# Kernel tuning notes

Measured on AMD Instinct MI355X. Metric: run time of the kernel, lower is better.

The kernel has to match this reference:

```python
import jax, jax.numpy as jnp
import numpy as np

N = 50000          # nodes
E = 400000         # edges
MUL = 32           # multiplicity per irrep
NUM_NEIGHBORS = 8.0
INV_SQRT3 = 1.0 / np.sqrt(3.0)  # w3j(1,1,0) coefficient


def setup_inputs() -> dict:
    key = jax.random.key(0)
    ks = jax.random.split(key, 20)
    inp = {
        # node_input: 32x0e (dim 32) + 32x1o (dim 96) = 128
        "node_input": jax.random.normal(ks[0], (N, 4 * MUL), jnp.float32),
        "node_attr": jnp.ones((N, 1), jnp.float32),           # 1x0e trivial attr
        "edge_src": jax.random.randint(ks[1], (E,), 0, N, jnp.int32),
        "edge_dst": jax.random.randint(ks[2], (E,), 0, N, jnp.int32),
        "edge_attr": jax.random.normal(ks[3], (E, 4), jnp.float32),   # 1x0e + 1x1o
        "edge_scalars": jax.random.normal(ks[4], (E, 16), jnp.float32),
        # FullyConnectedTensorProduct weights (uvw, node_attr has mul 1)
        "w_sc0": jax.random.normal(ks[5], (MUL, MUL), jnp.float32),
        "w_sc1": jax.random.normal(ks[6], (MUL, MUL), jnp.float32),
        "w_lin1_0": jax.random.normal(ks[7], (MUL, MUL), jnp.float32),
        "w_lin1_1": jax.random.normal(ks[8], (MUL, MUL), jnp.float32),
        # radial FC net -> per-edge TP weights (numel = 4*MUL = 128)
        "fc_w1": jax.random.normal(ks[9], (16, 64), jnp.float32),
        "fc_w2": jax.random.normal(ks[10], (64, 4 * MUL), jnp.float32),
        # lin2: irreps_mid (64x0e+64x1o) x attr -> output
        "w_lin2_0": jax.random.normal(ks[11], (2 * MUL, MUL), jnp.float32),
        "w_lin2_1": jax.random.normal(ks[12], (2 * MUL, MUL), jnp.float32),
        # alpha: irreps_mid x attr -> 0e (zero-init in original; small randn for a nontrivial test)
        "w_alpha": 0.1 * jax.random.normal(ks[13], (2 * MUL, 1), jnp.float32),
        # sc_edges: irreps_mid x edge_attr -> edge_attr
        "w_se0a": jax.random.normal(ks[14], (2 * MUL,), jnp.float32),  # mid0e x ea0e -> 0e
        "w_se0b": jax.random.normal(ks[15], (2 * MUL,), jnp.float32),  # mid1o x ea1o -> 0e
        "w_se1a": jax.random.normal(ks[16], (2 * MUL,), jnp.float32),  # mid0e x ea1o -> 1o
        "w_se1b": jax.random.normal(ks[17], (2 * MUL,), jnp.float32),  # mid1o x ea0e -> 1o
    }
    return inp


def reference(node_input, node_attr, edge_src, edge_dst, edge_attr, edge_scalars,
              w_sc0, w_sc1, w_lin1_0, w_lin1_1, fc_w1, fc_w2,
              w_lin2_0, w_lin2_1, w_alpha, w_se0a, w_se0b, w_se1a, w_se1b):
    inv_nn = 1.0 / jnp.sqrt(jnp.asarray(NUM_NEIGHBORS, node_input.dtype))
    n = node_input.shape[0]
    x0 = node_input[:, :MUL]                       # (N, 32)   32x0e
    x1 = node_input[:, MUL:].reshape(n, MUL, 3)    # (N, 32, 3) 32x1o
    a = node_attr                                  # (N, 1)
    s_in = 1.0 / np.sqrt(MUL)                      # FCTP fan-in normalization

    # self-connection: FCTP(input, attr) -> output
    sc0 = (x0 @ w_sc0) * a * s_in
    sc1 = jnp.einsum('num,uw->nwm', x1, w_sc1) * a[:, :, None] * s_in
    node_self = jnp.concatenate([sc0, sc1.reshape(n, 3 * MUL)], axis=1)  # (N, 128)

    # lin1: FCTP(input, attr) -> input irreps
    f0 = (x0 @ w_lin1_0) * a * s_in
    f1 = jnp.einsum('num,uw->nwm', x1, w_lin1_1) * a[:, :, None] * s_in

    # gather source node features per edge
    g0 = f0[edge_src]                              # (E, 32)
    g1 = f1[edge_src]                              # (E, 32, 3)
    ea0 = edge_attr[:, :1]                         # (E, 1)   1x0e
    ea1 = edge_attr[:, 1:]                         # (E, 3)   1x1o

    # radial net -> per-edge TP weights (FullyConnectedNet with sin activation)
    h = jnp.sin(edge_scalars @ fc_w1 * (1.0 / np.sqrt(16.0)))
    w = h @ fc_w2 * (1.0 / np.sqrt(64.0))          # (E, 128)
    wA, wB, wC, wD = jnp.split(w, 4, axis=1)       # each (E, 32)

    # uvu tensor product, 4 instructions
    mA = wA * g0 * ea0                                           # 0e x 0e -> 0e
    mD = wD * jnp.einsum('eum,em->eu', g1, ea1) * INV_SQRT3      # 1o x 1o -> 0e
    mB = (wB * g0)[:, :, None] * ea1[:, None, :]                 # 0e x 1o -> 1o
    mC = (wC[:, :, None] * g1) * ea0[:, :, None]                 # 1o x 0e -> 1o
    mid0 = jnp.concatenate([mA, mD], axis=1)       # (E, 64)  64x0e
    mid1 = jnp.concatenate([mB, mC], axis=1)       # (E, 64, 3) 64x1o

    # scatter-add to destination nodes
    n0 = jax.ops.segment_sum(mid0, edge_dst, num_segments=n) * inv_nn
    n1 = jax.ops.segment_sum(mid1, edge_dst, num_segments=n) * inv_nn

    s_mid = 1.0 / np.sqrt(2 * MUL)
    out0 = (n0 @ w_lin2_0) * a * s_mid
    out1 = jnp.einsum('num,uw->nwm', n1, w_lin2_1) * a[:, :, None] * s_mid
    node_conv = jnp.concatenate([out0, out1.reshape(n, 3 * MUL)], axis=1)

    # alpha gate (sc.output_mask is all ones here, so alpha = 1 - 1 + alpha*1)
    alpha = (n0 @ w_alpha) * a * s_mid             # (N, 1)
    node_conv_out = node_self + alpha * node_conv  # (N, 128)

    # sc_edges: FCTP(mid, edge_attr) -> edge_attr irreps; fan-in = 128 per output
    s_se = 1.0 / np.sqrt(4 * MUL)
    se0 = ((mid0 @ w_se0a) * ea0[:, 0]
           + jnp.einsum('eum,em,u->e', mid1, ea1, w_se0b) * INV_SQRT3) * s_se
    se1 = ((mid0 @ w_se1a)[:, None] * ea1
           + jnp.einsum('eum,u->em', mid1, w_se1b) * ea0) * s_se
    edge_conv_out = edge_attr + jnp.concatenate([se0[:, None], se1], axis=1) * inv_nn

    return node_conv_out, edge_conv_out
```

## Files before the change

kernel.cpp:

```cpp
#include <hip/hip_runtime.h>
#include <math.h>

#define N_NODES 50000
#define E_EDGES 400000
#define NPRE_BLOCKS 6250
#define NHIST_BLOCKS 1563
#define NEDGE_BLOCKS 6250

typedef _Float16 f16x2 __attribute__((ext_vector_type(2)));
typedef _Float16 f16x4 __attribute__((ext_vector_type(4)));
typedef _Float16 f16x8 __attribute__((ext_vector_type(8)));
typedef float    f32x4 __attribute__((ext_vector_type(4)));

static constexpr float S_IN      = 0.17677669529663687f;
static constexpr float S_MID     = 0.125f;
static constexpr float S_SE      = 0.08838834764831843f;
static constexpr float INV_NN    = 0.35355339059327373f;
static constexpr float INV_SQRT3 = 0.5773502691896258f;
static constexpr float FC1_S     = 0.25f;
static constexpr float FC2_S     = 0.125f;

#define WAVE_LDS_FENCE() asm volatile("s_waitcnt lgkmcnt(0)" ::: "memory")

__device__ inline float wave_reduce_dpp(float v) {
    int x;
    x = __builtin_amdgcn_update_dpp(0, __float_as_int(v), 0x111, 0xf, 0xf, true); v += __int_as_float(x);
    x = __builtin_amdgcn_update_dpp(0, __float_as_int(v), 0x112, 0xf, 0xf, true); v += __int_as_float(x);
    x = __builtin_amdgcn_update_dpp(0, __float_as_int(v), 0x114, 0xf, 0xf, true); v += __int_as_float(x);
    x = __builtin_amdgcn_update_dpp(0, __float_as_int(v), 0x118, 0xf, 0xf, true); v += __int_as_float(x);
    x = __builtin_amdgcn_update_dpp(0, __float_as_int(v), 0x142, 0xa, 0xf, true); v += __int_as_float(x);
    x = __builtin_amdgcn_update_dpp(0, __float_as_int(v), 0x143, 0xc, 0xf, true); v += __int_as_float(x);
    return __int_as_float(__builtin_amdgcn_readlane(__float_as_int(v), 63));
}

__global__ __launch_bounds__(256) void pre_hist_kernel(
    const float* __restrict__ node_input, const float* __restrict__ node_attr,
    const float* __restrict__ w_sc0, const float* __restrict__ w_sc1,
    const float* __restrict__ w_lin1_0, const float* __restrict__ w_lin1_1,
    float* __restrict__ out_self, _Float16* __restrict__ ws_h,
    const int* __restrict__ edge_dst, int* __restrict__ counts,
    const float* __restrict__ edge_scalars, _Float16* __restrict__ ES_h,
    float* __restrict__ nacc)
{
    const int t = threadIdx.x;
    if (blockIdx.x >= NPRE_BLOCKS) {
        const int e = (blockIdx.x - NPRE_BLOCKS) * 256 + t;
        if (e < E_EDGES) {
            atomicAdd(&counts[edge_dst[e]], 1);
            const float4* s4 = (const float4*)edge_scalars + (size_t)e * 4;
            _Float16* dp = ES_h + (size_t)e * 16;
            #pragma unroll
            for (int i = 0; i < 4; ++i) {
                const float4 v = s4[i];
                f16x4 p = {(_Float16)v.x, (_Float16)v.y, (_Float16)v.z, (_Float16)v.w};
                *(f16x4*)&dp[i * 4] = p;
            }
        }
        return;
    }
    const int n0 = blockIdx.x * 8;
    __shared__ __align__(16) float sx[8 * 128];
    __shared__ float sa[8];
    {
        const int k = t >> 5, q = t & 31;
        const float4 v = ((const float4*)(node_input + (size_t)n0 * 128))[t];
        if (q < 8) {
            *(float4*)&sx[k * 128 + q * 4] = v;
        } else {
            const int base = q * 4 - 32;
            const float vv[4] = {v.x, v.y, v.z, v.w};
            #pragma unroll
            for (int j = 0; j < 4; ++j) {
                const int uj = (base + j) / 3, mj = (base + j) % 3;
                sx[k * 128 + 32 + mj * 32 + uj] = vv[j];
            }
        }
    }
    {
        float4* nz = (float4*)(nacc + (size_t)n0 * 256);
        const float4 z4 = {0.f, 0.f, 0.f, 0.f};
        nz[t] = z4; nz[t + 256] = z4;
    }
    if (t < 8) sa[t] = node_attr[n0 + t];
    __syncthreads();

    const int half = t >> 7;
    const int idx  = t & 127;
    float wcol[32];
    int xoff = 0;
    if (idx < 32) {
        const float* __restrict__ W = half ? w_lin1_0 : w_sc0;
        #pragma unroll
        for (int u = 0; u < 32; ++u) wcol[u] = W[u * 32 + idx];
    } else {
        const float* __restrict__ W = half ? w_lin1_1 : w_sc1;
        const int j = idx - 32;
        const int w = j / 3; const int m = j % 3;
        xoff = 32 + m * 32;
        #pragma unroll
        for (int u = 0; u < 32; ++u) wcol[u] = W[u * 32 + w];
    }
    #pragma unroll
    for (int k = 0; k < 8; ++k) {
        const float* xb = sx + k * 128 + xoff;
        float acc = 0.f;
        #pragma unroll
        for (int u4 = 0; u4 < 8; ++u4) {
            const f32x4 xv = *(const f32x4*)&xb[u4 * 4];
            acc += xv[0] * wcol[u4 * 4 + 0];
            acc += xv[1] * wcol[u4 * 4 + 1];
            acc += xv[2] * wcol[u4 * 4 + 2];
            acc += xv[3] * wcol[u4 * 4 + 3];
        }
        const float v = acc * sa[k] * S_IN;
        if (half) ws_h[(size_t)(n0 + k) * 128 + idx] = (_Float16)v;
        else      out_self[(size_t)(n0 + k) * 128 + idx] = v;
    }
}

__global__ __launch_bounds__(1024) void scan_block_kernel(
    const int* __restrict__ counts, int* __restrict__ cursor, int* __restrict__ bsum,
    const float* __restrict__ fc_w1, const float* __restrict__ fc_w2,
    const float* __restrict__ w_se0a, const float* __restrict__ w_se0b,
    const float* __restrict__ w_se1a, const float* __restrict__ w_se1b,
    _Float16* __restrict__ W2T_g, _Float16* __restrict__ W1T_g,
    _Float16* __restrict__ BT_g)
{
    const int t = threadIdx.x;
    if (blockIdx.x == 49) {
        for (int u = t; u < 8192; u += 1024) {
            const int k = u >> 7, c = u & 127;
            W2T_g[c * 72 + k] = (_Float16)fc_w2[u];
        }
        {
            W2T_g[(t >> 3) * 72 + 64 + (t & 7)] = (_Float16)0.f;
        }
        {
            const int j = t >> 4, k = t & 15;
            W1T_g[t] = (_Float16)fc_w1[k * 64 + j];
        }
        for (int u = t; u < 2112; u += 1024) BT_g[u] = (_Float16)0.f;
        __syncthreads();
        if (t < 256) {
            const int uu = t & 63, p = t >> 6;
            const float ev = (p == 0) ? w_se0a[uu] : w_se1b[uu];
            const float ov = (p == 0) ? w_se1a[uu] : w_se0b[uu];
            BT_g[(2 * p) * 264 + 4 * uu + p]     = (_Float16)ev;
            BT_g[(2 * p + 1) * 264 + 4 * uu + p] = (_Float16)ov;
        }
        return;
    }
    const int idx = blockIdx.x * 1024 + t;
    const int c   = (idx < N_NODES) ? counts[idx] : 0;
    int v = c, x;
    x = __builtin_amdgcn_update_dpp(0, v, 0x111, 0xf, 0xf, true); v += x;
    x = __builtin_amdgcn_update_dpp(0, v, 0x112, 0xf, 0xf, true); v += x;
    x = __builtin_amdgcn_update_dpp(0, v, 0x114, 0xf, 0xf, true); v += x;
    x = __builtin_amdgcn_update_dpp(0, v, 0x118, 0xf, 0xf, true); v += x;
    x = __builtin_amdgcn_update_dpp(0, v, 0x142, 0xa, 0xf, true); v += x;
    x = __builtin_amdgcn_update_dpp(0, v, 0x143, 0xc, 0xf, true); v += x;
    __shared__ int swv[16], sex[16];
    const int wid = t >> 6;
    if ((t & 63) == 63) swv[wid] = v;
    __syncthreads();
    if (t < 16) {
        int a = 0;
        for (int j = 0; j < t; ++j) a += swv[j];
        sex[t] = a;
        if (t == 15) bsum[blockIdx.x] = a + swv[15];
    }
    __syncthreads();
    if (idx < N_NODES) cursor[idx] = v - c + sex[wid];
}

__global__ __launch_bounds__(1024) void scan_fixup_kernel(
    int* __restrict__ cursor, const int* __restrict__ bsum)
{
    __shared__ int boff_s;
    const int t = threadIdx.x;
    if (t < 64) {
        int v = (t < (int)blockIdx.x) ? bsum[t] : 0;
        #pragma unroll
        for (int off = 32; off >= 1; off >>= 1) v += __shfl_down(v, off, 64);
        if (t == 0) boff_s = v;
    }
    __syncthreads();
    const int idx = blockIdx.x * 1024 + t;
    if (idx < N_NODES) cursor[idx] += boff_s;
}

__global__ __launch_bounds__(256) void scatter_kernel(
    const int* __restrict__ edge_dst, int* __restrict__ cursor,
    int* __restrict__ sorted_eid)
{
    const int e = blockIdx.x * 256 + threadIdx.x;
    if (e < E_EDGES) {
        const int p = atomicAdd(&cursor[edge_dst[e]], 1);
        sorted_eid[p] = e;
    }
}

__global__ __launch_bounds__(256, 5) void edge_kernel(
    const _Float16* __restrict__ ws_h,
    const int* __restrict__ edge_src, const int* __restrict__ edge_dst,
    const float* __restrict__ edge_attr, const _Float16* __restrict__ ES_h,
    const _Float16* __restrict__ W2T_g, const _Float16* __restrict__ W1T_g,
    const _Float16* __restrict__ BT_g,
    const int* __restrict__ sorted_eid,
    float* __restrict__ nacc, float* __restrict__ edge_out)
{
    __shared__ __align__(16) _Float16 sArena[13056];
    __shared__ __align__(16) float sDep[4][36];

    _Float16* __restrict__ sHT = sArena;
    _Float16* __restrict__ sWt = sArena + 4608;

    const int t    = threadIdx.x;
    const int lane = t & 63;
    const int wv   = t >> 6;
    const int quad = lane >> 4;
    const int mm   = lane & 15;

    const int orig = blockIdx.x;
    const int xcd  = orig & 7;
    constexpr int q = NEDGE_BLOCKS >> 3, r = NEDGE_BLOCKS & 7;
    const int bid = (xcd < r ? xcd * (q + 1) : r * (q + 1) + (xcd - r) * q) + (orig >> 3);
    const int e0 = bid * 64;
    const int eb = wv * 16;

    int eidreg = 0, srcreg = 0, dstreg = 0;
    float4 ear = {0.f, 0.f, 0.f, 0.f};
    if (lane < 16) {
        eidreg = sorted_eid[e0 + eb + lane];
        srcreg = edge_src[eidreg];
        dstreg = edge_dst[eidreg];
        ear    = ((const float4*)edge_attr)[eidreg];
    }

    f16x8 a_w1[4];
    f16x8 b_es = {};
    if (quad < 2) {
        const int myeid = __shfl(eidreg, mm);
        b_es = *(const f16x8*)&ES_h[(size_t)myeid * 16 + quad * 8];
        #pragma unroll
        for (int jt = 0; jt < 4; ++jt)
            a_w1[jt] = *(const f16x8*)&W1T_g[(jt * 16 + mm) * 16 + quad * 8];
    } else {
        #pragma unroll
        for (int jt = 0; jt < 4; ++jt) a_w1[jt] = (f16x8){};
    }

    const bool hi = lane >= 32;
    const int  u  = lane - 32;
    const int idxA = hi ? (32 + 3 * u) : lane;
    const int idxB = hi ? (33 + 3 * u) : lane;
    const int idxC = hi ? (34 + 3 * u) : lane;
    const int col1 = hi ? (96 + u) : lane;
    const int col2 = hi ? (64 + u) : (32 + lane);

    float ga[2][4], gb[2][4], gc[2][4];
    #pragma unroll
    for (int b = 0; b < 2; ++b)
        #pragma unroll
        for (int i = 0; i < 4; ++i) {
            const int s = __shfl(srcreg, b * 4 + i);
            const _Float16* fr = ws_h + (size_t)s * 128;
            ga[b][i] = (float)fr[idxA];
            gb[b][i] = (float)fr[idxB];
            gc[b][i] = (float)fr[idxC];
        }
    asm volatile("" ::: "memory");

    #pragma unroll
    for (int jt = 0; jt < 4; ++jt) {
        f32x4 d = {0.f, 0.f, 0.f, 0.f};
        d = __builtin_amdgcn_mfma_f32_16x16x32_f16(a_w1[jt], b_es, d, 0, 0, 0);
        f16x4 hv;
        hv[0] = (_Float16)__sinf(d[0] * FC1_S);
        hv[1] = (_Float16)__sinf(d[1] * FC1_S);
        hv[2] = (_Float16)__sinf(d[2] * FC1_S);
        hv[3] = (_Float16)__sinf(d[3] * FC1_S);
        *(f16x4*)&sHT[(eb + mm) * 72 + jt * 16 + quad * 4] = hv;
    }
    WAVE_LDS_FENCE();

    f32x4 dacc[8];
    {
        const f16x8 b_lo = *(const f16x8*)&sHT[(eb + mm) * 72 + quad * 8];
        const f16x8 b_hi = *(const f16x8*)&sHT[(eb + mm) * 72 + 32 + quad * 8];
        #pragma unroll
        for (int ct = 0; ct < 8; ++ct) {
            const f16x8 a_lo = *(const f16x8*)&W2T_g[(ct * 16 + mm) * 72 + quad * 8];
            const f16x8 a_hi = *(const f16x8*)&W2T_g[(ct * 16 + mm) * 72 + 32 + quad * 8];
            f32x4 d = {0.f, 0.f, 0.f, 0.f};
            d = __builtin_amdgcn_mfma_f32_16x16x32_f16(a_lo, b_lo, d, 0, 0, 0);
            d = __builtin_amdgcn_mfma_f32_16x16x32_f16(a_hi, b_hi, d, 0, 0, 0);
            dacc[ct] = d;
        }
    }

    #pragma unroll
    for (int ct = 0; ct < 8; ++ct) {
        f16x4 v;
        v[0] = (_Float16)(dacc[ct][0] * FC2_S);
        v[1] = (_Float16)(dacc[ct][1] * FC2_S);
        v[2] = (_Float16)(dacc[ct][2] * FC2_S);
        v[3] = (_Float16)(dacc[ct][3] * FC2_S);
        *(f16x4*)&sWt[(eb + mm) * 132 + ct * 16 + quad * 4] = v;
    }
    WAVE_LDS_FENCE();

    int   cur = -1;
    float am0 = 0.f, axx = 0.f, ayy = 0.f, azz = 0.f;
    _Float16* __restrict__ myA = sArena + wv * 1152;
    const _Float16* __restrict__ arow = myA + (mm & 3) * 264;
    const _Float16* __restrict__ btrow = BT_g + (mm & 7) * 264;

    #pragma unroll
    for (int b = 0; b < 4; ++b) {
        const int sl = b & 1;
        float w1b[4], w2b[4];
        #pragma unroll
        for (int i = 0; i < 4; ++i) {
            w1b[i] = (float)sWt[(eb + b * 4 + i) * 132 + col1];
            w2b[i] = (float)sWt[(eb + b * 4 + i) * 132 + col2];
        }
        #pragma unroll
        for (int i = 0; i < 4; ++i) {
            const int el = b * 4 + i;
            const int dst = __shfl(dstreg, el);
            const float ea0 = __shfl(ear.x, el);
            const float e1x = __shfl(ear.y, el);
            const float e1y = __shfl(ear.z, el);
            const float e1z = __shfl(ear.w, el);
            const float w1v = w1b[i];
            const float w2v = w2b[i];

            float mid0, m1x, m1y, m1z;
            if (!hi) {
                mid0 = w1v * ga[sl][i] * ea0;
                const float wbg = w2v * ga[sl][i];
                m1x = wbg * e1x; m1y = wbg * e1y; m1z = wbg * e1z;
            } else {
                const float dot = ga[sl][i] * e1x + gb[sl][i] * e1y + gc[sl][i] * e1z;
                mid0 = w1v * dot * INV_SQRT3;
                const float wce = w2v * ea0;
                m1x = wce * ga[sl][i]; m1y = wce * gb[sl][i]; m1z = wce * gc[sl][i];
            }

            if (dst != cur) {
                if (cur >= 0) {
                    float* np_ = nacc + (size_t)cur * 256;
                    atomicAdd(np_ + lane, am0);
                    atomicAdd(np_ + 64 + lane, axx);
                    atomicAdd(np_ + 128 + lane, ayy);
                    atomicAdd(np_ + 192 + lane, azz);
                }
                cur = dst; am0 = axx = ayy = azz = 0.f;
            }
            am0 += mid0; axx += m1x; ayy += m1y; azz += m1z;

            f16x4 mv;
            mv[0] = (_Float16)mid0; mv[1] = (_Float16)m1x;
            mv[2] = (_Float16)m1y;  mv[3] = (_Float16)m1z;
            *(f16x4*)&myA[i * 264 + 4 * lane] = mv;
        }

        if (b < 2) {
            #pragma unroll
            for (int i = 0; i < 4; ++i) {
                const int s = __shfl(srcreg, (b + 2) * 4 + i);
                const _Float16* fr = ws_h + (size_t)s * 128;
                ga[sl][i] = (float)fr[idxA];
                gb[sl][i] = (float)fr[idxB];
                gc[sl][i] = (float)fr[idxC];
            }
            asm volatile("" ::: "memory");
        }

        f32x4 d = {0.f, 0.f, 0.f, 0.f};
        #pragma unroll
        for (int ks = 0; ks < 8; ++ks) {
            const f16x8 a  = *(const f16x8*)&arow[ks * 32 + quad * 8];
            const f16x8 bb = *(const f16x8*)&btrow[ks * 32 + quad * 8];
            d = __builtin_amdgcn_mfma_f32_16x16x32_f16(a, bb, d, 0, 0, 0);
        }
        if (lane < 8) {
            float4 f4; f4.x = d[0]; f4.y = d[1]; f4.z = d[2]; f4.w = d[3];
            *(float4*)&sDep[wv][lane * 4] = f4;
        }
        const int oeid = __shfl(eidreg, b * 4 + (lane & 3));
        const float oea0 = __shfl(ear.x, b * 4 + (lane & 3));
        const float oe1x = __shfl(ear.y, b * 4 + (lane & 3));
        const float oe1y = __shfl(ear.z, b * 4 + (lane & 3));
        const float oe1z = __shfl(ear.w, b * 4 + (lane & 3));
        if (lane < 4) {
            const float c0 = sDep[wv][ 0 + lane], c1 = sDep[wv][ 4 + lane];
            const float c2 = sDep[wv][ 8 + lane], c3 = sDep[wv][12 + lane];
            const float c4 = sDep[wv][16 + lane], c5 = sDep[wv][20 + lane];
            const float c6 = sDep[wv][24 + lane], c7 = sDep[wv][28 + lane];
            const float s0 = c0 * oea0 + (c3 * oe1x + c5 * oe1y + c7 * oe1z) * INV_SQRT3;
            float4 o;
            o.x = oea0 + s0 * S_SE * INV_NN;
            o.y = oe1x + (c1 * oe1x + c2 * oea0) * S_SE * INV_NN;
            o.z = oe1y + (c1 * oe1y + c4 * oea0) * S_SE * INV_NN;
            o.w = oe1z + (c1 * oe1z + c6 * oea0) * S_SE * INV_NN;
            *(float4*)&edge_out[(size_t)oeid * 4] = o;
        }
    }
    if (cur >= 0) {
        float* np_ = nacc + (size_t)cur * 256;
        atomicAdd(np_ + lane, am0);
        atomicAdd(np_ + 64 + lane, axx);
        atomicAdd(np_ + 128 + lane, ayy);
        atomicAdd(np_ + 192 + lane, azz);
    }
}

__global__ __launch_bounds__(128) void node_post_kernel(
    const float* __restrict__ nacc, const float* __restrict__ node_attr,
    const float* __restrict__ w_lin2_0, const float* __restrict__ w_lin2_1,
    const float* __restrict__ w_alpha, float* __restrict__ out)
{
    const int n0 = blockIdx.x * 8, t = threadIdx.x;
    __shared__ __align__(16) float sn[8 * 256];
    __shared__ float salpha[8];
    const float4* src = (const float4*)(nacc + (size_t)n0 * 256);
    #pragma unroll
    for (int i = 0; i < 4; ++i) ((float4*)sn)[t + i * 128] = src[t + i * 128];
    __syncthreads();

    if (t < 64) {
        const float wa = w_alpha[t];
        #pragma unroll
        for (int k = 0; k < 8; ++k) {
            const float r = wave_reduce_dpp(sn[k * 256 + t] * wa);
            if (t == 0) salpha[k] = r;
        }
    }
    __syncthreads();

    float wcol[64];
    int xoff = 0;
    if (t < 32) {
        #pragma unroll
        for (int u = 0; u < 64; ++u) wcol[u] = w_lin2_0[u * 32 + t];
    } else {
        const int j = t - 32; const int w = j / 3; const int m = j % 3;
        xoff = 64 + m * 64;
        #pragma unroll
        for (int u = 0; u < 64; ++u) wcol[u] = w_lin2_1[u * 32 + w];
    }
    #pragma unroll
    for (int k = 0; k < 8; ++k) {
        const float* xb = sn + k * 256 + xoff;
        float acc = 0.f;
        #pragma unroll
        for (int u4 = 0; u4 < 16; ++u4) {
            const f32x4 xv = *(const f32x4*)&xb[u4 * 4];
            acc += xv[0] * wcol[u4 * 4 + 0];
            acc += xv[1] * wcol[u4 * 4 + 1];
            acc += xv[2] * wcol[u4 * 4 + 2];
            acc += xv[3] * wcol[u4 * 4 + 3];
        }
        const float a  = node_attr[n0 + k];
        const float sc = a * S_MID * INV_NN;
        const size_t o = (size_t)(n0 + k) * 128 + t;
        out[o] = out[o] + (salpha[k] * sc) * (acc * sc);
    }
}

extern "C" void kernel_launch(void* const* d_in, const int* in_sizes, int n_in,
                              void* d_out, int out_size, void* d_ws, size_t ws_size,
                              hipStream_t stream)
{
    const float* node_input   = (const float*)d_in[0];
    const float* node_attr    = (const float*)d_in[1];
    const int*   edge_src     = (const int*)d_in[2];
    const int*   edge_dst     = (const int*)d_in[3];
    const float* edge_attr    = (const float*)d_in[4];
    const float* edge_scalars = (const float*)d_in[5];
    const float* w_sc0        = (const float*)d_in[6];
    const float* w_sc1        = (const float*)d_in[7];
    const float* w_lin1_0     = (const float*)d_in[8];
    const float* w_lin1_1     = (const float*)d_in[9];
    const float* fc_w1        = (const float*)d_in[10];
    const float* fc_w2        = (const float*)d_in[11];
    const float* w_lin2_0     = (const float*)d_in[12];
    const float* w_lin2_1     = (const float*)d_in[13];
    const float* w_alpha      = (const float*)d_in[14];
    const float* w_se0a       = (const float*)d_in[15];
    const float* w_se0b       = (const float*)d_in[16];
    const float* w_se1a       = (const float*)d_in[17];
    const float* w_se1b       = (const float*)d_in[18];

    float* out      = (float*)d_out;
    float* edge_out = out + (size_t)N_NODES * 128;

    _Float16* ws_h = (_Float16*)d_ws;
    _Float16* ES_h = ws_h + (size_t)N_NODES * 128;
    float* nacc   = (float*)((char*)d_ws + (size_t)N_NODES * 128 * 4);
    int*   counts = (int*)(nacc + (size_t)N_NODES * 256);
    int*   cursor = counts + N_NODES;
    int*   sid    = cursor + N_NODES;
    int*   bsum   = sid + E_EDGES;
    _Float16* W2T_g = (_Float16*)(bsum + 64);
    _Float16* W1T_g = W2T_g + 9216;
    _Float16* BT_g  = W1T_g + 1024;

    hipMemsetAsync(counts, 0, N_NODES * sizeof(int), stream);

    pre_hist_kernel<<<NPRE_BLOCKS + NHIST_BLOCKS, 256, 0, stream>>>(
        node_input, node_attr, w_sc0, w_sc1, w_lin1_0, w_lin1_1, out, ws_h,
        edge_dst, counts, edge_scalars, ES_h, nacc);

    scan_block_kernel<<<50, 1024, 0, stream>>>(counts, cursor, bsum,
        fc_w1, fc_w2, w_se0a, w_se0b, w_se1a, w_se1b, W2T_g, W1T_g, BT_g);
    scan_fixup_kernel<<<49, 1024, 0, stream>>>(cursor, bsum);
    scatter_kernel<<<(E_EDGES + 255) / 256, 256, 0, stream>>>(edge_dst, cursor, sid);

    edge_kernel<<<NEDGE_BLOCKS, 256, 0, stream>>>(
        ws_h, edge_src, edge_dst, edge_attr, ES_h, W2T_g, W1T_g, BT_g,
        sid, nacc, edge_out);

    node_post_kernel<<<N_NODES / 8, 128, 0, stream>>>(
        nacc, node_attr, w_lin2_0, w_lin2_1, w_alpha, out);
}
```

Measured before the change: 373.2 us.

## Fuse scan, fixup and scatter into one kernel with grid-wide barriers

Replaces the three counting-sort kernels (block scan, scan fixup, scatter) with one persistent kernel of 128 blocks that uses atomic-counter grid barriers between phases. The aim is to remove two kernel launches and their inter-kernel gaps. The scatter phase becomes a grid-stride loop over 128×1024 threads. This relies on all 128 blocks being co-resident, otherwise the barrier deadlocks. It also raises the edge_kernel occupancy hint from 5 to 6 waves per SIMD, which may increase register pressure or spilling.

```diff
diff --git a/kernel.cpp b/kernel.cpp
--- a/kernel.cpp
+++ b/kernel.cpp
@@ -6,6 +6,7 @@
 #define NPRE_BLOCKS 6250
 #define NHIST_BLOCKS 1563
 #define NEDGE_BLOCKS 6250
+#define NFUSE_BLOCKS 128
 
 typedef _Float16 f16x2 __attribute__((ext_vector_type(2)));
 typedef _Float16 f16x4 __attribute__((ext_vector_type(4)));
@@ -33,6 +34,17 @@
     return __int_as_float(__builtin_amdgcn_readlane(__float_as_int(v), 63));
 }
 
+__device__ inline void gsync(int* cnt, int target) {
+    __syncthreads();
+    if (threadIdx.x == 0) {
+        __hip_atomic_fetch_add(cnt, 1, __ATOMIC_ACQ_REL, __HIP_MEMORY_SCOPE_AGENT);
+        while (__hip_atomic_load(cnt, __ATOMIC_ACQUIRE, __HIP_MEMORY_SCOPE_AGENT) < target)
+            __builtin_amdgcn_s_sleep(8);
+    }
+    __syncthreads();
+    __threadfence();
+}
+
 __global__ __launch_bounds__(256) void pre_hist_kernel(
     const float* __restrict__ node_input, const float* __restrict__ node_attr,
     const float* __restrict__ w_sc0, const float* __restrict__ w_sc1,
@@ -40,9 +52,10 @@
     float* __restrict__ out_self, _Float16* __restrict__ ws_h,
     const int* __restrict__ edge_dst, int* __restrict__ counts,
     const float* __restrict__ edge_scalars, _Float16* __restrict__ ES_h,
-    float* __restrict__ nacc)
+    float* __restrict__ nacc, int* __restrict__ sync_cnt)
 {
     const int t = threadIdx.x;
+    if (blockIdx.x == 0 && t == 0) *sync_cnt = 0;
     if (blockIdx.x >= NPRE_BLOCKS) {
         const int e = (blockIdx.x - NPRE_BLOCKS) * 256 + t;
         if (e < E_EDGES) {
@@ -118,16 +131,43 @@
     }
 }
 
-__global__ __launch_bounds__(1024) void scan_block_kernel(
-    const int* __restrict__ counts, int* __restrict__ cursor, int* __restrict__ bsum,
+__global__ __launch_bounds__(1024) void sort_fused_kernel(
+    const int* __restrict__ edge_dst, const int* __restrict__ counts,
+    int* __restrict__ cursor, int* __restrict__ bsum,
+    int* __restrict__ sorted_eid, int* __restrict__ sync_cnt,
     const float* __restrict__ fc_w1, const float* __restrict__ fc_w2,
     const float* __restrict__ w_se0a, const float* __restrict__ w_se0b,
     const float* __restrict__ w_se1a, const float* __restrict__ w_se1b,
     _Float16* __restrict__ W2T_g, _Float16* __restrict__ W1T_g,
     _Float16* __restrict__ BT_g)
 {
-    const int t = threadIdx.x;
-    if (blockIdx.x == 49) {
+    const int t = threadIdx.x, b = blockIdx.x;
+    const int idx = b * 1024 + t;
+    __shared__ int swv[16], sex[16];
+    __shared__ int boff_s;
+    int myexc = 0;
+
+    if (b < 49) {
+        const int c = (idx < N_NODES) ? counts[idx] : 0;
+        int v = c, x;
+        x = __builtin_amdgcn_update_dpp(0, v, 0x111, 0xf, 0xf, true); v += x;
+        x = __builtin_amdgcn_update_dpp(0, v, 0x112, 0xf, 0xf, true); v += x;
+        x = __builtin_amdgcn_update_dpp(0, v, 0x114, 0xf, 0xf, true); v += x;
+        x = __builtin_amdgcn_update_dpp(0, v, 0x118, 0xf, 0xf, true); v += x;
+        x = __builtin_amdgcn_update_dpp(0, v, 0x142, 0xa, 0xf, true); v += x;
+        x = __builtin_amdgcn_update_dpp(0, v, 0x143, 0xc, 0xf, true); v += x;
+        const int wid = t >> 6;
+        if ((t & 63) == 63) swv[wid] = v;
+        __syncthreads();
+        if (t < 16) {
+            int a = 0;
+            for (int j = 0; j < t; ++j) a += swv[j];
+            sex[t] = a;
+            if (t == 15) bsum[b] = a + swv[15];
+        }
+        __syncthreads();
+        myexc = v - c + sex[wid];
+    } else if (b == 127) {
         for (int u = t; u < 8192; u += 1024) {
             const int k = u >> 7, c = u & 127;
             W2T_g[c * 72 + k] = (_Float16)fc_w2[u];
@@ -148,59 +188,28 @@
             BT_g[(2 * p) * 264 + 4 * uu + p]     = (_Float16)ev;
             BT_g[(2 * p + 1) * 264 + 4 * uu + p] = (_Float16)ov;
         }
-        return;
-    }
-    const int idx = blockIdx.x * 1024 + t;
-    const int c   = (idx < N_NODES) ? counts[idx] : 0;
-    int v = c, x;
-    x = __builtin_amdgcn_update_dpp(0, v, 0x111, 0xf, 0xf, true); v += x;
-    x = __builtin_amdgcn_update_dpp(0, v, 0x112, 0xf, 0xf, true); v += x;
-    x = __builtin_amdgcn_update_dpp(0, v, 0x114, 0xf, 0xf, true); v += x;
-    x = __builtin_amdgcn_update_dpp(0, v, 0x118, 0xf, 0xf, true); v += x;
-    x = __builtin_amdgcn_update_dpp(0, v, 0x142, 0xa, 0xf, true); v += x;
-    x = __builtin_amdgcn_update_dpp(0, v, 0x143, 0xc, 0xf, true); v += x;
-    __shared__ int swv[16], sex[16];
-    const int wid = t >> 6;
-    if ((t & 63) == 63) swv[wid] = v;
-    __syncthreads();
-    if (t < 16) {
-        int a = 0;
-        for (int j = 0; j < t; ++j) a += swv[j];
-        sex[t] = a;
-        if (t == 15) bsum[blockIdx.x] = a + swv[15];
-    }
-    __syncthreads();
-    if (idx < N_NODES) cursor[idx] = v - c + sex[wid];
-}
-
-__global__ __launch_bounds__(1024) void scan_fixup_kernel(
-    int* __restrict__ cursor, const int* __restrict__ bsum)
-{
-    __shared__ int boff_s;
-    const int t = threadIdx.x;
-    if (t < 64) {
-        int v = (t < (int)blockIdx.x) ? bsum[t] : 0;
-        #pragma unroll
-        for (int off = 32; off >= 1; off >>= 1) v += __shfl_down(v, off, 64);
-        if (t == 0) boff_s = v;
-    }
-    __syncthreads();
-    const int idx = blockIdx.x * 1024 + t;
-    if (idx < N_NODES) cursor[idx] += boff_s;
-}
-
-__global__ __launch_bounds__(256) void scatter_kernel(
-    const int* __restrict__ edge_dst, int* __restrict__ cursor,
-    int* __restrict__ sorted_eid)
-{
-    const int e = blockIdx.x * 256 + threadIdx.x;
-    if (e < E_EDGES) {
+    }
+    gsync(sync_cnt, 1 * NFUSE_BLOCKS);
+
+    if (b < 49) {
+        if (t < 64) {
+            int vv = (t < b) ? bsum[t] : 0;
+            #pragma unroll
+            for (int off = 32; off >= 1; off >>= 1) vv += __shfl_down(vv, off, 64);
+            if (t == 0) boff_s = vv;
+        }
+        __syncthreads();
+        if (idx < N_NODES) cursor[idx] = myexc + boff_s;
+    }
+    gsync(sync_cnt, 2 * NFUSE_BLOCKS);
+
+    for (int e = idx; e < E_EDGES; e += NFUSE_BLOCKS * 1024) {
         const int p = atomicAdd(&cursor[edge_dst[e]], 1);
         sorted_eid[p] = e;
     }
 }
 
-__global__ __launch_bounds__(256, 5) void edge_kernel(
+__global__ __launch_bounds__(256, 6) void edge_kernel(
     const _Float16* __restrict__ ws_h,
     const int* __restrict__ edge_src, const int* __restrict__ edge_dst,
     const float* __restrict__ edge_attr, const _Float16* __restrict__ ES_h,
@@ -507,17 +516,17 @@
     _Float16* W2T_g = (_Float16*)(bsum + 64);
     _Float16* W1T_g = W2T_g + 9216;
     _Float16* BT_g  = W1T_g + 1024;
+    int* sync_cnt   = (int*)(BT_g + 2112);
 
     hipMemsetAsync(counts, 0, N_NODES * sizeof(int), stream);
 
     pre_hist_kernel<<<NPRE_BLOCKS + NHIST_BLOCKS, 256, 0, stream>>>(
         node_input, node_attr, w_sc0, w_sc1, w_lin1_0, w_lin1_1, out, ws_h,
-        edge_dst, counts, edge_scalars, ES_h, nacc);
-
-    scan_block_kernel<<<50, 1024, 0, stream>>>(counts, cursor, bsum,
+        edge_dst, counts, edge_scalars, ES_h, nacc, sync_cnt);
+
+    sort_fused_kernel<<<NFUSE_BLOCKS, 1024, 0, stream>>>(
+        edge_dst, counts, cursor, bsum, sid, sync_cnt,
         fc_w1, fc_w2, w_se0a, w_se0b, w_se1a, w_se1b, W2T_g, W1T_g, BT_g);
-    scan_fixup_kernel<<<49, 1024, 0, stream>>>(cursor, bsum);
-    scatter_kernel<<<(E_EDGES + 255) / 256, 256, 0, stream>>>(edge_dst, cursor, sid);
 
     edge_kernel<<<NEDGE_BLOCKS, 256, 0, stream>>>(
         ws_h, edge_src, edge_dst, edge_attr, ES_h, W2T_g, W1T_g, BT_g,
```

Result: slower. 510.3 us (+36.7%).
